# Optimization experiments

Hardware: AMD Instinct MI355X
Metric: run time of the kernel (lower is better)

Reference implementation:

```python
import jax, jax.numpy as jnp
import numpy as np

D = 1024
FFN = 1024
EPS_LN = 1e-5
EPS_GN = 1e-5

def _ln(x, w, b):
    m = x.mean(-1, keepdims=True)
    v = x.var(-1, keepdims=True)
    return (x - m) / jnp.sqrt(v + EPS_LN) * w + b

def setup_inputs() -> dict:
    key = jax.random.key(0)
    ks = jax.random.split(key, 24)
    p = lambda i, shp, s=0.02: jax.random.normal(ks[i], shp, jnp.float32) * s
    inp = {
        'x': jax.random.normal(ks[0], (8, 2048, D), jnp.float32),
        'state': jnp.zeros((8, D), jnp.float32),
        'ln1_w': jnp.ones((D,)), 'ln1_b': jnp.zeros((D,)),
        'ln2_w': jnp.ones((D,)), 'ln2_b': jnp.zeros((D,)),
        'gn_w': jnp.ones((D,)), 'gn_b': jnp.zeros((D,)),
        'grn_gamma': jnp.zeros((1, 1, D)), 'grn_beta': jnp.zeros((1, 1, D)),
        'decay': jnp.full((D,), -3.0, jnp.float32),
        'Wr': p(1, (D, D), 0.05), 'Wk': p(2, (D, D)), 'Wv': p(3, (D, D)),
        'Wg': p(4, (D, D), 0.05), 'Wa': p(5, (D, D)), 'Wb': p(6, (D, D)),
        'Wout': p(7, (D, D)), 'Wffnout': p(8, (D, D)),
        'Wfk': p(9, (D, FFN)), 'bfk': jnp.zeros((FFN,)),
        'Wfv': p(10, (FFN, D)), 'bfv': jnp.zeros((D,)),
        'Wfr': p(11, (D, D)), 'bfr': jnp.zeros((D,)),
    }
    return inp

def reference(x, state, ln1_w, ln1_b, ln2_w, ln2_b, gn_w, gn_b, grn_gamma, grn_beta, decay, Wr, Wk, Wv, Wg, Wa, Wb, Wout, Wffnout, Wfk, bfk, Wfv, bfv, Wfr, bfr):
    B, T, Dd = x.shape
    xx = _ln(x, ln1_w, ln1_b)
    shifted = jnp.pad(xx, ((0, 0), (1, 0), (0, 0)))[:, :-1]  # ZeroPad2d((0,0,1,-1))
    xm = 0.5 * (xx + shifted)
    r = xm @ Wr
    k = xm @ Wk
    v = xm @ Wv
    a = xm @ Wa
    b = xm @ Wb
    g = jax.nn.sigmoid(xm @ Wg)
    w = jnp.exp(-jnp.exp(decay))  # [D]
    u = k * v + a * b  # [B,T,D]
    def step(s, ut):
        s = s * w + ut
        return s, s
    final_state, states = jax.lax.scan(step, state, jnp.swapaxes(u, 0, 1))
    states = jnp.swapaxes(states, 0, 1)  # [B,T,D]
    # GroupNorm(dim//32, dim) applied over flattened (B*T, D)
    G = Dd // 32
    s4 = states.reshape(B, T, G, 32)
    m = s4.mean(-1, keepdims=True)
    va = s4.var(-1, keepdims=True)
    norm_states = ((s4 - m) / jnp.sqrt(va + EPS_GN)).reshape(B, T, Dd) * gn_w + gn_b
    mixed_out = (jax.nn.sigmoid(r) * norm_states * g) @ Wout
    x = x + mixed_out  # dropout is identity at inference
    xx2 = _ln(x, ln2_w, ln2_b)
    k_ffn = jnp.square(jax.nn.relu(xx2 @ Wfk + bfk))
    h = k_ffn @ Wfv + bfv  # [B,T,D]
    # GRN: L2 norm over time dim (dim=1), mean over channels
    gx = jnp.sqrt(jnp.sum(h * h, axis=1, keepdims=True))  # [B,1,D]
    nx = gx / (gx.mean(-1, keepdims=True) + 1e-6)
    ffn_hidden = grn_gamma * (h * nx) + grn_beta + h
    ffn_out = (jax.nn.sigmoid(xx2 @ Wfr + bfr) * ffn_hidden) @ Wffnout
    x = x + ffn_out
    return (x, final_state)
```

## Files before the change

kernel.cpp:

```cpp
#include <hip/hip_runtime.h>
#include <hip/hip_bf16.h>
#include <math.h>

#define D_DIM 1024
#define T_DIM 2048
#define B_DIM 8
#define M_DIM (B_DIM * T_DIM)
#define SZ ((size_t)M_DIM * D_DIM)
#define NW 11
#define CCH 16
#define LCH 128
#define GCH 32
#define GLCH 64

typedef __bf16 bf16_t;
typedef __bf16 bf16x8 __attribute__((ext_vector_type(8)));
typedef __bf16 bf16x4 __attribute__((ext_vector_type(4)));
typedef float f32x4 __attribute__((ext_vector_type(4)));

typedef const __attribute__((address_space(1))) void* as1_const_ptr;
typedef __attribute__((address_space(3))) void* as3_ptr;

__device__ __forceinline__ void load_lds_16(const void* g, void* l) {
    __builtin_amdgcn_global_load_lds((as1_const_ptr)g, (as3_ptr)l, 16, 0, 0);
}

__device__ __forceinline__ float sigmoid_f(float x) { return 1.f / (1.f + expf(-x)); }

template<int NT, int MODE>
__global__ void __launch_bounds__(256)
gemm2_kernel(const bf16_t* __restrict__ A, const bf16_t* __restrict__ Bt,
             void* __restrict__ out0, void* __restrict__ out1,
             const float* __restrict__ bias0, const float* __restrict__ bias1,
             const void* __restrict__ other)
{
    constexpr int K = D_DIM;
    __shared__ bf16_t sA[2][128 * 32];
    __shared__ bf16_t sB[2][128 * 32];
    const int tid  = threadIdx.x;
    const int wave = tid >> 6, lane = tid & 63;

    const int lin = blockIdx.x;
    const int xcd = lin & 7;
    const int idx = lin >> 3;
    const int mt  = xcd * 16 + idx / NT;
    const int nt  = idx % NT;
    const int m0 = mt * 128, n0 = nt * 128;

    const int wm = (wave & 1) * 64, wn = (wave >> 1) * 64;

    const int rl = lane >> 2;
    const int cc = lane & 3;
    const int scol = (cc ^ ((rl >> 1) & 3)) * 8;
    const int srow = wave * 32 + rl;
    const bf16_t* gA = A  + (size_t)(m0 + srow) * K + scol;
    const bf16_t* gB = Bt + (size_t)(n0 + srow) * K + scol;
    const int lofs = (wave * 32) * 32;

    f32x4 acc[4][4] = {};

    const int fr = lane & 15;
    const int quad = lane >> 4;
    const int qs = (quad ^ ((fr >> 1) & 3)) * 8;

    load_lds_16(gA,                   &sA[0][lofs]);
    load_lds_16(gA + (size_t)16 * K,  &sA[0][lofs + 16 * 32]);
    load_lds_16(gB,                   &sB[0][lofs]);
    load_lds_16(gB + (size_t)16 * K,  &sB[0][lofs + 16 * 32]);
    __syncthreads();

    int cur = 0;
    for (int kk = 0; kk < K; kk += 32) {
        if (kk + 32 < K) {
            const int nb = cur ^ 1;
            load_lds_16(gA + kk + 32,                   &sA[nb][lofs]);
            load_lds_16(gA + (size_t)16 * K + kk + 32,  &sA[nb][lofs + 16 * 32]);
            load_lds_16(gB + kk + 32,                   &sB[nb][lofs]);
            load_lds_16(gB + (size_t)16 * K + kk + 32,  &sB[nb][lofs + 16 * 32]);
        }
        bf16x8 af[4], bq[4];
        #pragma unroll
        for (int i = 0; i < 4; i++)
            af[i] = *(const bf16x8*)(&sA[cur][(wm + i * 16 + fr) * 32 + qs]);
        #pragma unroll
        for (int j = 0; j < 4; j++)
            bq[j] = *(const bf16x8*)(&sB[cur][(wn + j * 16 + fr) * 32 + qs]);
        #pragma unroll
        for (int i = 0; i < 4; i++)
            #pragma unroll
            for (int j = 0; j < 4; j++)
                acc[i][j] = __builtin_amdgcn_mfma_f32_16x16x32_bf16(af[i], bq[j], acc[i][j], 0, 0, 0);
        __syncthreads();
        cur ^= 1;
    }

    #pragma unroll
    for (int i = 0; i < 4; i++) {
        #pragma unroll
        for (int j = 0; j < 4; j++) {
            const int col = n0 + wn + j * 16 + fr;
            #pragma unroll
            for (int r = 0; r < 4; r++) {
                const int row = m0 + wm + i * 16 + quad * 4 + r;
                float v = acc[i][j][r];
                if constexpr (MODE == 0) {
                    ((float*)out0)[(size_t)row * D_DIM + col] = v + bias0[col];
                } else if constexpr (MODE == 3) {
                    const size_t id = (size_t)row * D_DIM + col;
                    ((float*)out0)[id] = v + ((const float*)other)[id];
                } else if constexpr (MODE == 5) {
                    const int w = nt >> 3;
                    const int lc = col & (D_DIM - 1);
                    const size_t id = (size_t)row * D_DIM + lc;
                    if (w == 0) {
                        float v2 = fmaxf(v + bias0[lc], 0.f);
                        ((bf16_t*)out0)[id] = (bf16_t)(v2 * v2);
                    } else {
                        ((bf16_t*)out1)[id] = (bf16_t)sigmoid_f(v + bias1[lc]);
                    }
                } else {
                    const int w = nt >> 3;
                    const size_t id = (size_t)row * D_DIM + (col & (D_DIM - 1));
                    if (w == 0) ((bf16_t*)out0)[id] = (bf16_t)sigmoid_f(v);
                    else        ((bf16_t*)out1)[id] = (bf16_t)sigmoid_f(v);
                }
            }
        }
    }
}

__global__ void __launch_bounds__(256, 2)
gemm_uv_kernel(const bf16_t* __restrict__ A, const bf16_t* __restrict__ Wt4,
               float* __restrict__ u)
{
    constexpr int K = D_DIM;
    constexpr size_t WSZ_E = (size_t)D_DIM * D_DIM;
    __shared__ bf16_t sA[2][128 * 32];
    __shared__ bf16_t sB[2][128 * 32];
    const int tid  = threadIdx.x;
    const int wave = tid >> 6, lane = tid & 63;

    const int lin = blockIdx.x;
    const int xcd = lin & 7;
    const int idx = lin >> 3;
    const int mt  = xcd * 16 + (idx >> 3);
    const int nt  = idx & 7;
    const int m0 = mt * 128, n0 = nt * 128;

    const int wm = (wave & 1) * 64, wn = (wave >> 1) * 64;

    const int rl = lane >> 2;
    const int cc = lane & 3;
    const int scol = (cc ^ ((rl >> 1) & 3)) * 8;
    const int srow = wave * 32 + rl;
    const bf16_t* gA  = A   + (size_t)(m0 + srow) * K + scol;
    const bf16_t* gB0 = Wt4 + (size_t)(n0 + srow) * K + scol;
    const int lofs = (wave * 32) * 32;

    const int fr = lane & 15;
    const int quad = lane >> 4;
    const int qs = (quad ^ ((fr >> 1) & 3)) * 8;

    auto kloop = [&](const bf16_t* gB, f32x4 (&acc)[4][4]) {
        load_lds_16(gA,                   &sA[0][lofs]);
        load_lds_16(gA + (size_t)16 * K,  &sA[0][lofs + 16 * 32]);
        load_lds_16(gB,                   &sB[0][lofs]);
        load_lds_16(gB + (size_t)16 * K,  &sB[0][lofs + 16 * 32]);
        __syncthreads();
        int cur = 0;
        for (int kk = 0; kk < K; kk += 32) {
            if (kk + 32 < K) {
                const int nb = cur ^ 1;
                load_lds_16(gA + kk + 32,                   &sA[nb][lofs]);
                load_lds_16(gA + (size_t)16 * K + kk + 32,  &sA[nb][lofs + 16 * 32]);
                load_lds_16(gB + kk + 32,                   &sB[nb][lofs]);
                load_lds_16(gB + (size_t)16 * K + kk + 32,  &sB[nb][lofs + 16 * 32]);
            }
            bf16x8 af[4], bq[4];
            #pragma unroll
            for (int i = 0; i < 4; i++)
                af[i] = *(const bf16x8*)(&sA[cur][(wm + i * 16 + fr) * 32 + qs]);
            #pragma unroll
            for (int j = 0; j < 4; j++)
                bq[j] = *(const bf16x8*)(&sB[cur][(wn + j * 16 + fr) * 32 + qs]);
            #pragma unroll
            for (int i = 0; i < 4; i++)
                #pragma unroll
                for (int j = 0; j < 4; j++)
                    acc[i][j] = __builtin_amdgcn_mfma_f32_16x16x32_bf16(af[i], bq[j], acc[i][j], 0, 0, 0);
            __syncthreads();
            cur ^= 1;
        }
    };

    f32x4 aKV[4][4] = {};
    f32x4 aT[4][4]  = {};
    f32x4 aB2[4][4] = {};

    kloop(gB0,              aKV);
    kloop(gB0 + WSZ_E,      aT);
    #pragma unroll
    for (int i = 0; i < 4; i++)
        #pragma unroll
        for (int j = 0; j < 4; j++) {
            aKV[i][j] = aKV[i][j] * aT[i][j];
            aT[i][j] = f32x4{0.f, 0.f, 0.f, 0.f};
        }
    kloop(gB0 + 2 * WSZ_E,  aT);
    kloop(gB0 + 3 * WSZ_E,  aB2);

    #pragma unroll
    for (int i = 0; i < 4; i++) {
        #pragma unroll
        for (int j = 0; j < 4; j++) {
            const int col = n0 + wn + j * 16 + fr;
            #pragma unroll
            for (int r = 0; r < 4; r++) {
                const int row = m0 + wm + i * 16 + quad * 4 + r;
                u[(size_t)row * D_DIM + col] =
                    aKV[i][j][r] + aT[i][j][r] * aB2[i][j][r];
            }
        }
    }
}

struct WList { const float* w[NW]; };

__global__ void __launch_bounds__(256)
transpose_cvt_kernel(WList wl, bf16_t* wt_base)
{
    __shared__ float tile[32][33];
    const float* W = wl.w[blockIdx.z];
    bf16_t* Wt = wt_base + (size_t)blockIdx.z * D_DIM * D_DIM;
    const int bx = blockIdx.x * 32, by = blockIdx.y * 32;
    const int tx = threadIdx.x, ty = threadIdx.y;
    #pragma unroll
    for (int i = 0; i < 32; i += 8)
        tile[ty + i][tx] = W[(size_t)(by + ty + i) * D_DIM + bx + tx];
    __syncthreads();
    #pragma unroll
    for (int i = 0; i < 32; i += 8)
        Wt[(size_t)(bx + ty + i) * D_DIM + by + tx] = (bf16_t)tile[tx][ty + i];
}

__global__ void __launch_bounds__(256)
ew_kernel(const float* __restrict__ decay, float* __restrict__ ew)
{
    const int d = blockIdx.x * 256 + threadIdx.x;
    if (d < D_DIM) ew[d] = expf(decay[d]);
}

__global__ void __launch_bounds__(256)
ln_shift_kernel(const float* __restrict__ x, const float* __restrict__ w,
                const float* __restrict__ bias, bf16_t* __restrict__ xm)
{
    const int row = blockIdx.x;
    const int t = row & (T_DIM - 1);
    const int d0 = threadIdx.x * 4;
    const float* xc = x + (size_t)row * D_DIM;
    f32x4 c = *(const f32x4*)(xc + d0);
    f32x4 p = {0.f, 0.f, 0.f, 0.f};
    if (t > 0) p = *(const f32x4*)(xc - D_DIM + d0);

    float sc = 0.f, qc = 0.f, sp = 0.f, qp = 0.f;
    #pragma unroll
    for (int e = 0; e < 4; e++) {
        sc += c[e]; qc += c[e] * c[e];
        sp += p[e]; qp += p[e] * p[e];
    }
    #pragma unroll
    for (int off = 32; off > 0; off >>= 1) {
        sc += __shfl_down(sc, off); qc += __shfl_down(qc, off);
        sp += __shfl_down(sp, off); qp += __shfl_down(qp, off);
    }
    __shared__ float red[16];
    const int wv = threadIdx.x >> 6, ln = threadIdx.x & 63;
    if (ln == 0) { red[wv] = sc; red[4 + wv] = qc; red[8 + wv] = sp; red[12 + wv] = qp; }
    __syncthreads();
    sc = red[0] + red[1] + red[2] + red[3];
    qc = red[4] + red[5] + red[6] + red[7];
    sp = red[8] + red[9] + red[10] + red[11];
    qp = red[12] + red[13] + red[14] + red[15];

    const float inv = 1.f / (float)D_DIM;
    const float mc = sc * inv, vc = qc * inv - mc * mc, rc = rsqrtf(vc + 1e-5f);
    const float mp = sp * inv, vp = qp * inv - mp * mp, rp = rsqrtf(vp + 1e-5f);

    bf16x4 o;
    #pragma unroll
    for (int e = 0; e < 4; e++) {
        const int d = d0 + e;
        const float wd = w[d], bd = bias[d];
        const float nc = (c[e] - mc) * rc * wd + bd;
        const float np = (t > 0) ? ((p[e] - mp) * rp * wd + bd) : 0.f;
        o[e] = (bf16_t)(0.5f * (nc + np));
    }
    *(bf16x4*)(xm + (size_t)row * D_DIM + d0) = o;
}

__global__ void __launch_bounds__(256)
scan1_kernel(float* __restrict__ u, const float* __restrict__ ew,
             float* __restrict__ carry)
{
    const int gid = blockIdx.x * 256 + threadIdx.x;
    const int d = gid & (D_DIM - 1);
    const int b = (gid >> 10) & (B_DIM - 1);
    const int c = gid >> 13;
    const float w = expf(-ew[d]);
    float s = 0.f;
    const size_t base = ((size_t)b * T_DIM + (size_t)c * LCH) * D_DIM + d;
    #pragma unroll 4
    for (int tl = 0; tl < LCH; tl++) {
        const size_t idx = base + (size_t)tl * D_DIM;
        s = fmaf(s, w, u[idx]);
        u[idx] = s;
    }
    carry[(size_t)(b * CCH + c) * D_DIM + d] = s;
}

__global__ void __launch_bounds__(256)
scan2_kernel(const float* __restrict__ s0, const float* __restrict__ ew,
             const float* __restrict__ carry, float* __restrict__ inc,
             float* __restrict__ fstate)
{
    const int gid = blockIdx.x * 256 + threadIdx.x;
    const int d = gid & (D_DIM - 1);
    const int b = gid >> 10;
    const float wL = expf(-(float)LCH * ew[d]);
    float s = s0[gid];
    #pragma unroll
    for (int c = 0; c < CCH; c++) {
        const size_t idx = (size_t)(b * CCH + c) * D_DIM + d;
        inc[idx] = s;
        s = fmaf(s, wL, carry[idx]);
    }
    fstate[gid] = s;
}

__global__ void __launch_bounds__(256)
mixed_kernel(const float* __restrict__ st, const float* __restrict__ inc,
             const float* __restrict__ ew, const bf16_t* __restrict__ sr,
             const bf16_t* __restrict__ g, const float* __restrict__ gnw,
             const float* __restrict__ gnb, bf16_t* __restrict__ outp)
{
    const int row = blockIdx.x;
    const int b = row >> 11;
    const int t = row & (T_DIM - 1);
    const int c = t >> 7, tl = t & (LCH - 1);
    const int d0 = threadIdx.x * 4;
    const size_t base = (size_t)row * D_DIM + d0;

    f32x4 lv = *(const f32x4*)(st + base);
    f32x4 iv = *(const f32x4*)(inc + (size_t)(b * CCH + c) * D_DIM + d0);
    f32x4 ev = *(const f32x4*)(ew + d0);

    float s[4];
    float sum = 0.f, sq = 0.f;
    #pragma unroll
    for (int e = 0; e < 4; e++) {
        s[e] = lv[e] + expf(-(float)(tl + 1) * ev[e]) * iv[e];
        sum += s[e]; sq += s[e] * s[e];
    }
    #pragma unroll
    for (int m = 1; m <= 4; m <<= 1) { sum += __shfl_xor(sum, m); sq += __shfl_xor(sq, m); }
    const float mean = sum * (1.f / 32.f);
    const float var  = sq * (1.f / 32.f) - mean * mean;
    const float rstd = rsqrtf(var + 1e-5f);

    bf16x4 rv = *(const bf16x4*)(sr + base);
    bf16x4 gv = *(const bf16x4*)(g + base);
    f32x4 wv = *(const f32x4*)(gnw + d0);
    f32x4 bv = *(const f32x4*)(gnb + d0);
    bf16x4 o;
    #pragma unroll
    for (int e = 0; e < 4; e++) {
        const float ns = (s[e] - mean) * rstd * wv[e] + bv[e];
        o[e] = (bf16_t)((float)rv[e] * ns * (float)gv[e]);
    }
    *(bf16x4*)(outp + base) = o;
}

__global__ void __launch_bounds__(256)
ln2_kernel(const float* __restrict__ x2, const float* __restrict__ w,
           const float* __restrict__ bias, bf16_t* __restrict__ xx2)
{
    const int row = blockIdx.x;
    const int d0 = threadIdx.x * 4;
    const float* xc = x2 + (size_t)row * D_DIM;
    f32x4 c = *(const f32x4*)(xc + d0);
    float sc = 0.f, qc = 0.f;
    #pragma unroll
    for (int e = 0; e < 4; e++) { sc += c[e]; qc += c[e] * c[e]; }
    #pragma unroll
    for (int off = 32; off > 0; off >>= 1) {
        sc += __shfl_down(sc, off); qc += __shfl_down(qc, off);
    }
    __shared__ float red[8];
    const int wv = threadIdx.x >> 6, ln = threadIdx.x & 63;
    if (ln == 0) { red[wv] = sc; red[4 + wv] = qc; }
    __syncthreads();
    sc = red[0] + red[1] + red[2] + red[3];
    qc = red[4] + red[5] + red[6] + red[7];
    const float inv = 1.f / (float)D_DIM;
    const float m = sc * inv, v = qc * inv - m * m, rs = rsqrtf(v + 1e-5f);
    bf16x4 o;
    #pragma unroll
    for (int e = 0; e < 4; e++) {
        const int d = d0 + e;
        o[e] = (bf16_t)((c[e] - m) * rs * w[d] + bias[d]);
    }
    *(bf16x4*)(xx2 + (size_t)row * D_DIM + d0) = o;
}

__global__ void __launch_bounds__(256)
grn1_kernel(const float* __restrict__ h, float* __restrict__ partial)
{
    const int blk = blockIdx.x;
    const int b = blk >> 5, c = blk & (GCH - 1);
    const int d0 = threadIdx.x * 4;
    const size_t base = ((size_t)b * T_DIM + (size_t)c * GLCH) * D_DIM + d0;
    f32x4 acc = {0.f, 0.f, 0.f, 0.f};
    for (int tl = 0; tl < GLCH; tl++) {
        f32x4 hv = *(const f32x4*)(h + base + (size_t)tl * D_DIM);
        #pragma unroll
        for (int e = 0; e < 4; e++) acc[e] = fmaf(hv[e], hv[e], acc[e]);
    }
    *(f32x4*)(partial + (size_t)blk * D_DIM + d0) = acc;
}

__global__ void __launch_bounds__(1024)
grn2_kernel(const float* __restrict__ partial, float* __restrict__ nx)
{
    const int b = blockIdx.x, d = threadIdx.x;
    float s = 0.f;
    #pragma unroll 4
    for (int c = 0; c < GCH; c++) s += partial[(size_t)(b * GCH + c) * D_DIM + d];
    const float gx = sqrtf(s);
    float v = gx;
    #pragma unroll
    for (int off = 32; off > 0; off >>= 1) v += __shfl_down(v, off);
    __shared__ float red[16];
    if ((threadIdx.x & 63) == 0) red[threadIdx.x >> 6] = v;
    __syncthreads();
    float tot = 0.f;
    #pragma unroll
    for (int i = 0; i < 16; i++) tot += red[i];
    nx[b * D_DIM + d] = gx / (tot * (1.f / (float)D_DIM) + 1e-6f);
}

__global__ void __launch_bounds__(256)
frh_kernel(const float* __restrict__ h, const bf16_t* __restrict__ fr,
           const float* __restrict__ nx, const float* __restrict__ gamma,
           const float* __restrict__ beta, bf16_t* __restrict__ outp)
{
    const size_t gid = (size_t)blockIdx.x * 256 + threadIdx.x;
    const size_t i4 = gid * 4;
    const int d = (int)(i4 & (D_DIM - 1));
    const int b = (int)(i4 >> 21);
    f32x4 hv = *(const f32x4*)(h + i4);
    bf16x4 fv = *(const bf16x4*)(fr + i4);
    f32x4 nv = *(const f32x4*)(nx + (size_t)b * D_DIM + d);
    f32x4 gm = *(const f32x4*)(gamma + d);
    f32x4 bt = *(const f32x4*)(beta + d);
    bf16x4 o;
    #pragma unroll
    for (int e = 0; e < 4; e++) {
        const float hh = hv[e];
        const float val = gm[e] * (hh * nv[e]) + bt[e] + hh;
        o[e] = (bf16_t)((float)fv[e] * val);
    }
    *(bf16x4*)(outp + i4) = o;
}

extern "C" void kernel_launch(void* const* d_in, const int* in_sizes, int n_in,
                              void* d_out, int out_size, void* d_ws, size_t ws_size,
                              hipStream_t stream)
{
    (void)in_sizes; (void)n_in; (void)out_size; (void)ws_size;

    const float* x      = (const float*)d_in[0];
    const float* state0 = (const float*)d_in[1];
    const float* ln1_w  = (const float*)d_in[2];
    const float* ln1_b  = (const float*)d_in[3];
    const float* ln2_w  = (const float*)d_in[4];
    const float* ln2_b  = (const float*)d_in[5];
    const float* gn_w   = (const float*)d_in[6];
    const float* gn_b   = (const float*)d_in[7];
    const float* grn_g  = (const float*)d_in[8];
    const float* grn_b  = (const float*)d_in[9];
    const float* decay  = (const float*)d_in[10];
    const float* bfk    = (const float*)d_in[20];
    const float* bfv    = (const float*)d_in[22];
    const float* bfr    = (const float*)d_in[24];

    const size_t WSZ = (size_t)D_DIM * D_DIM;
    float*  F1 = (float*)d_ws;
    bf16_t* B0 = (bf16_t*)(F1 + SZ);
    bf16_t* B1 = B0 + SZ;
    bf16_t* B2 = B1 + SZ;
    bf16_t* B3 = B2 + SZ;
    bf16_t* WT = B3 + SZ;
    float*  carry   = (float*)(WT + NW * WSZ);
    float*  inc     = carry + (size_t)B_DIM * CCH * D_DIM;
    float*  partial = inc + (size_t)B_DIM * CCH * D_DIM;
    float*  nxp     = partial + (size_t)B_DIM * GCH * D_DIM;
    float*  ewp     = nxp + (size_t)B_DIM * D_DIM;

    WList wl;
    const int widx[NW] = {11, 14, 12, 13, 15, 16, 17, 19, 23, 21, 18};
    for (int i = 0; i < NW; i++) wl.w[i] = (const float*)d_in[widx[i]];

    float* out_x  = (float*)d_out;
    float* out_st = out_x + SZ;

    transpose_cvt_kernel<<<dim3(32, 32, NW), dim3(32, 8), 0, stream>>>(wl, WT);
    ew_kernel<<<4, 256, 0, stream>>>(decay, ewp);
    ln_shift_kernel<<<M_DIM, 256, 0, stream>>>(x, ln1_w, ln1_b, B0);

    gemm2_kernel<16, 6><<<8 * 16 * 16, 256, 0, stream>>>(
        B0, WT + 0 * WSZ, B2, B3, nullptr, nullptr, nullptr);
    gemm_uv_kernel<<<8 * 16 * 8, 256, 0, stream>>>(B0, WT + 2 * WSZ, F1);

    scan1_kernel<<<(CCH * B_DIM * D_DIM) / 256, 256, 0, stream>>>(F1, ewp, carry);
    scan2_kernel<<<(B_DIM * D_DIM) / 256, 256, 0, stream>>>(state0, ewp, carry, inc, out_st);
    mixed_kernel<<<M_DIM, 256, 0, stream>>>(F1, inc, ewp, B2, B3, gn_w, gn_b, B1);

    gemm2_kernel<8, 3><<<8 * 16 * 8, 256, 0, stream>>>(
        B1, WT + 6 * WSZ, out_x, nullptr, nullptr, nullptr, x);
    ln2_kernel<<<M_DIM, 256, 0, stream>>>(out_x, ln2_w, ln2_b, B0);

    gemm2_kernel<16, 5><<<8 * 16 * 16, 256, 0, stream>>>(
        B0, WT + 7 * WSZ, B1, B2, bfk, bfr, nullptr);
    gemm2_kernel<8, 0><<<8 * 16 * 8, 256, 0, stream>>>(
        B1, WT + 9 * WSZ, F1, nullptr, bfv, nullptr, nullptr);

    grn1_kernel<<<B_DIM * GCH, 256, 0, stream>>>(F1, partial);
    grn2_kernel<<<B_DIM, 1024, 0, stream>>>(partial, nxp);
    frh_kernel<<<M_DIM, 256, 0, stream>>>(F1, B2, nxp, grn_g, grn_b, B3);

    gemm2_kernel<8, 3><<<8 * 16 * 8, 256, 0, stream>>>(
        B3, WT + 10 * WSZ, out_x, nullptr, nullptr, nullptr, out_x);
}
```

Baseline: 991.9 us.

## Enlarge GEMM tiles to 256x128 with 512 threads and fuse GRN sum-of-squares

The generic GEMM kernel now uses 512-thread blocks with 256x128 output tiles, so the A and B tiles are split differently across waves and grid sizes are halved. The FFN value projection epilogue (new mode 7) accumulates per-column sums of squares and writes per-tile partials, which removes the separate grn1 pass that re-read h. grn2 now reduces 8 partials per batch instead of 32. The intent is better operand reuse per block and one fewer full read of h, at the cost of more LDS per block and different occupancy.

```diff
diff --git a/kernel.cpp b/kernel.cpp
--- a/kernel.cpp
+++ b/kernel.cpp
@@ -10,8 +10,6 @@
 #define NW 11
 #define CCH 16
 #define LCH 128
-#define GCH 32
-#define GLCH 64
 
 typedef __bf16 bf16_t;
 typedef __bf16 bf16x8 __attribute__((ext_vector_type(8)));
@@ -28,34 +26,36 @@
 __device__ __forceinline__ float sigmoid_f(float x) { return 1.f / (1.f + expf(-x)); }
 
 template<int NT, int MODE>
-__global__ void __launch_bounds__(256)
+__global__ void __launch_bounds__(512, 4)
 gemm2_kernel(const bf16_t* __restrict__ A, const bf16_t* __restrict__ Bt,
              void* __restrict__ out0, void* __restrict__ out1,
              const float* __restrict__ bias0, const float* __restrict__ bias1,
              const void* __restrict__ other)
 {
     constexpr int K = D_DIM;
-    __shared__ bf16_t sA[2][128 * 32];
+    __shared__ bf16_t sA[2][256 * 32];
     __shared__ bf16_t sB[2][128 * 32];
+    __shared__ float gsum[8][64];
     const int tid  = threadIdx.x;
     const int wave = tid >> 6, lane = tid & 63;
 
     const int lin = blockIdx.x;
     const int xcd = lin & 7;
     const int idx = lin >> 3;
-    const int mt  = xcd * 16 + idx / NT;
+    const int mt  = xcd * 8 + idx / NT;
     const int nt  = idx % NT;
-    const int m0 = mt * 128, n0 = nt * 128;
-
-    const int wm = (wave & 1) * 64, wn = (wave >> 1) * 64;
+    const int m0 = mt * 256, n0 = nt * 128;
+
+    const int wm = (wave & 3) * 64;
+    const int wn = (wave >> 2) * 64;
 
     const int rl = lane >> 2;
     const int cc = lane & 3;
     const int scol = (cc ^ ((rl >> 1) & 3)) * 8;
-    const int srow = wave * 32 + rl;
-    const bf16_t* gA = A  + (size_t)(m0 + srow) * K + scol;
-    const bf16_t* gB = Bt + (size_t)(n0 + srow) * K + scol;
-    const int lofs = (wave * 32) * 32;
+    const bf16_t* gA = A  + (size_t)(m0 + wave * 32 + rl) * K + scol;
+    const bf16_t* gB = Bt + (size_t)(n0 + wave * 16 + rl) * K + scol;
+    const int lofsA = (wave * 32) * 32;
+    const int lofsB = (wave * 16) * 32;
 
     f32x4 acc[4][4] = {};
 
@@ -63,20 +63,18 @@
     const int quad = lane >> 4;
     const int qs = (quad ^ ((fr >> 1) & 3)) * 8;
 
-    load_lds_16(gA,                   &sA[0][lofs]);
-    load_lds_16(gA + (size_t)16 * K,  &sA[0][lofs + 16 * 32]);
-    load_lds_16(gB,                   &sB[0][lofs]);
-    load_lds_16(gB + (size_t)16 * K,  &sB[0][lofs + 16 * 32]);
+    load_lds_16(gA,                   &sA[0][lofsA]);
+    load_lds_16(gA + (size_t)16 * K,  &sA[0][lofsA + 16 * 32]);
+    load_lds_16(gB,                   &sB[0][lofsB]);
     __syncthreads();
 
     int cur = 0;
     for (int kk = 0; kk < K; kk += 32) {
         if (kk + 32 < K) {
             const int nb = cur ^ 1;
-            load_lds_16(gA + kk + 32,                   &sA[nb][lofs]);
-            load_lds_16(gA + (size_t)16 * K + kk + 32,  &sA[nb][lofs + 16 * 32]);
-            load_lds_16(gB + kk + 32,                   &sB[nb][lofs]);
-            load_lds_16(gB + (size_t)16 * K + kk + 32,  &sB[nb][lofs + 16 * 32]);
+            load_lds_16(gA + kk + 32,                   &sA[nb][lofsA]);
+            load_lds_16(gA + (size_t)16 * K + kk + 32,  &sA[nb][lofsA + 16 * 32]);
+            load_lds_16(gB + kk + 32,                   &sB[nb][lofsB]);
         }
         bf16x8 af[4], bq[4];
         #pragma unroll
@@ -94,6 +92,8 @@
         cur ^= 1;
     }
 
+    float hs[4] = {0.f, 0.f, 0.f, 0.f};
+
     #pragma unroll
     for (int i = 0; i < 4; i++) {
         #pragma unroll
@@ -103,9 +103,7 @@
             for (int r = 0; r < 4; r++) {
                 const int row = m0 + wm + i * 16 + quad * 4 + r;
                 float v = acc[i][j][r];
-                if constexpr (MODE == 0) {
-                    ((float*)out0)[(size_t)row * D_DIM + col] = v + bias0[col];
-                } else if constexpr (MODE == 3) {
+                if constexpr (MODE == 3) {
                     const size_t id = (size_t)row * D_DIM + col;
                     ((float*)out0)[id] = v + ((const float*)other)[id];
                 } else if constexpr (MODE == 5) {
@@ -118,13 +116,34 @@
                     } else {
                         ((bf16_t*)out1)[id] = (bf16_t)sigmoid_f(v + bias1[lc]);
                     }
-                } else {
+                } else if constexpr (MODE == 6) {
                     const int w = nt >> 3;
                     const size_t id = (size_t)row * D_DIM + (col & (D_DIM - 1));
                     if (w == 0) ((bf16_t*)out0)[id] = (bf16_t)sigmoid_f(v);
                     else        ((bf16_t*)out1)[id] = (bf16_t)sigmoid_f(v);
+                } else {
+                    const float h = v + bias0[col];
+                    ((float*)out0)[(size_t)row * D_DIM + col] = h;
+                    hs[j] += h * h;
                 }
             }
+        }
+    }
+
+    if constexpr (MODE == 7) {
+        #pragma unroll
+        for (int j = 0; j < 4; j++) {
+            float t = hs[j];
+            t += __shfl_xor(t, 16);
+            t += __shfl_xor(t, 32);
+            if (lane < 16) gsum[wave][j * 16 + fr] = t;
+        }
+        __syncthreads();
+        if (tid < 128) {
+            const int p = tid >> 6, jf = tid & 63;
+            const float tot = gsum[4 * p + 0][jf] + gsum[4 * p + 1][jf]
+                            + gsum[4 * p + 2][jf] + gsum[4 * p + 3][jf];
+            ((float*)out1)[(size_t)mt * D_DIM + n0 + p * 64 + jf] = tot;
         }
     }
 }
@@ -412,29 +431,13 @@
     *(bf16x4*)(xx2 + (size_t)row * D_DIM + d0) = o;
 }
 
-__global__ void __launch_bounds__(256)
-grn1_kernel(const float* __restrict__ h, float* __restrict__ partial)
-{
-    const int blk = blockIdx.x;
-    const int b = blk >> 5, c = blk & (GCH - 1);
-    const int d0 = threadIdx.x * 4;
-    const size_t base = ((size_t)b * T_DIM + (size_t)c * GLCH) * D_DIM + d0;
-    f32x4 acc = {0.f, 0.f, 0.f, 0.f};
-    for (int tl = 0; tl < GLCH; tl++) {
-        f32x4 hv = *(const f32x4*)(h + base + (size_t)tl * D_DIM);
-        #pragma unroll
-        for (int e = 0; e < 4; e++) acc[e] = fmaf(hv[e], hv[e], acc[e]);
-    }
-    *(f32x4*)(partial + (size_t)blk * D_DIM + d0) = acc;
-}
-
 __global__ void __launch_bounds__(1024)
 grn2_kernel(const float* __restrict__ partial, float* __restrict__ nx)
 {
     const int b = blockIdx.x, d = threadIdx.x;
     float s = 0.f;
-    #pragma unroll 4
-    for (int c = 0; c < GCH; c++) s += partial[(size_t)(b * GCH + c) * D_DIM + d];
+    #pragma unroll
+    for (int c = 0; c < 8; c++) s += partial[(size_t)(b * 8 + c) * D_DIM + d];
     const float gx = sqrtf(s);
     float v = gx;
     #pragma unroll
@@ -503,7 +506,7 @@
     float*  carry   = (float*)(WT + NW * WSZ);
     float*  inc     = carry + (size_t)B_DIM * CCH * D_DIM;
     float*  partial = inc + (size_t)B_DIM * CCH * D_DIM;
-    float*  nxp     = partial + (size_t)B_DIM * GCH * D_DIM;
+    float*  nxp     = partial + (size_t)64 * D_DIM;
     float*  ewp     = nxp + (size_t)B_DIM * D_DIM;
 
     WList wl;
@@ -517,27 +520,26 @@
     ew_kernel<<<4, 256, 0, stream>>>(decay, ewp);
     ln_shift_kernel<<<M_DIM, 256, 0, stream>>>(x, ln1_w, ln1_b, B0);
 
-    gemm2_kernel<16, 6><<<8 * 16 * 16, 256, 0, stream>>>(
+    gemm2_kernel<16, 6><<<1024, 512, 0, stream>>>(
         B0, WT + 0 * WSZ, B2, B3, nullptr, nullptr, nullptr);
-    gemm_uv_kernel<<<8 * 16 * 8, 256, 0, stream>>>(B0, WT + 2 * WSZ, F1);
+    gemm_uv_kernel<<<1024, 256, 0, stream>>>(B0, WT + 2 * WSZ, F1);
 
     scan1_kernel<<<(CCH * B_DIM * D_DIM) / 256, 256, 0, stream>>>(F1, ewp, carry);
     scan2_kernel<<<(B_DIM * D_DIM) / 256, 256, 0, stream>>>(state0, ewp, carry, inc, out_st);
     mixed_kernel<<<M_DIM, 256, 0, stream>>>(F1, inc, ewp, B2, B3, gn_w, gn_b, B1);
 
-    gemm2_kernel<8, 3><<<8 * 16 * 8, 256, 0, stream>>>(
+    gemm2_kernel<8, 3><<<512, 512, 0, stream>>>(
         B1, WT + 6 * WSZ, out_x, nullptr, nullptr, nullptr, x);
     ln2_kernel<<<M_DIM, 256, 0, stream>>>(out_x, ln2_w, ln2_b, B0);
 
-    gemm2_kernel<16, 5><<<8 * 16 * 16, 256, 0, stream>>>(
+    gemm2_kernel<16, 5><<<1024, 512, 0, stream>>>(
         B0, WT + 7 * WSZ, B1, B2, bfk, bfr, nullptr);
-    gemm2_kernel<8, 0><<<8 * 16 * 8, 256, 0, stream>>>(
-        B1, WT + 9 * WSZ, F1, nullptr, bfv, nullptr, nullptr);
-
-    grn1_kernel<<<B_DIM * GCH, 256, 0, stream>>>(F1, partial);
+    gemm2_kernel<8, 7><<<512, 512, 0, stream>>>(
+        B1, WT + 9 * WSZ, F1, partial, bfv, nullptr, nullptr);
+
     grn2_kernel<<<B_DIM, 1024, 0, stream>>>(partial, nxp);
     frh_kernel<<<M_DIM, 256, 0, stream>>>(F1, B2, nxp, grn_g, grn_b, B3);
 
-    gemm2_kernel<8, 3><<<8 * 16 * 8, 256, 0, stream>>>(
+    gemm2_kernel<8, 3><<<512, 512, 0, stream>>>(
         B3, WT + 10 * WSZ, out_x, nullptr, nullptr, nullptr, out_x);
 }
```

Measured after the change: 926.4 us. -6.6%, faster.
